# Optimization experiments

Hardware: AMD Instinct MI355X
Metric: run time of the kernel (lower is better)

## Reference

```python
import jax, jax.numpy as jnp
import numpy as np

B, L, D, G = 4, 4096, 2048, 32
GS = D // G  # group size
EPS = 1e-05


def setup_inputs() -> dict:
    key = jax.random.key(0)
    kx, = jax.random.split(key, 1)
    return {
        "x": jax.random.normal(kx, (B, L, D), dtype=jnp.float32),
        "prev_count": jnp.zeros((B,), dtype=jnp.int32),
        "prev_mean": jnp.zeros((B, G), dtype=jnp.float32),
        "prev_var": jnp.ones((B, G), dtype=jnp.float32),
        "padding_mask": jnp.ones((B, L), dtype=jnp.bool_),
        "weight": jnp.ones((D,), dtype=jnp.float32),
        "bias": jnp.zeros((D,), dtype=jnp.float32),
    }


def _timestep_norm(x, prev_count, prev_mean, prev_var, padding_mask, weight, bias):
    b, l, d = x.shape
    xg = x.reshape(b, l, G, GS).transpose(1, 0, 2, 3)  # (L, B, G, GS)
    mk = padding_mask.transpose(1, 0)                   # (L, B)
    w = weight.reshape(1, G, GS)
    bi = bias.reshape(1, G, GS)

    def step(carry, inp):
        count, mean, var = carry            # (B,), (B,G), (B,G)
        x_t, mask_t = inp                   # (B,G,GS), (B,)
        m_t = x_t.mean(axis=-1)             # per-group mean at this timestep, (B,G)
        valid = mask_t.astype(jnp.float32)[:, None]
        c_new = count + mask_t.astype(count.dtype)
        c_safe = jnp.maximum(c_new, 1).astype(jnp.float32)[:, None]
        delta = m_t - mean
        mean = mean + delta * valid / c_safe
        m2 = var * jnp.maximum(count, 1).astype(jnp.float32)[:, None]
        m2 = m2 + delta * (m_t - mean) * valid  # Welford second-moment update
        var = m2 / c_safe
        x_hat = (x_t - mean[..., None]) * jax.lax.rsqrt(var[..., None] + EPS)
        y_t = x_hat * w + bi
        return (c_new, mean, var), y_t

    (count, mean, var), ys = jax.lax.scan(step, (prev_count, prev_mean, prev_var), (xg, mk))
    y = ys.transpose(1, 0, 2, 3).reshape(b, l, d)
    return y, count, mean, var


def reference(x, prev_count, prev_mean, prev_var, padding_mask, weight, bias):
    return _timestep_norm(x, prev_count, prev_mean, prev_var, padding_mask, weight, bias)
```

## Files before the change

kernel.cpp:

```cpp
#include <hip/hip_runtime.h>

namespace {
constexpr int Bc  = 4;
constexpr int Lc  = 4096;
constexpr int Dc  = 2048;
constexpr int Gc  = 32;
constexpr int GSc = 64;
constexpr int CH  = 16;
constexpr int CT  = Lc / CH;
constexpr float EPSc = 1e-5f;
constexpr long long NY = (long long)Bc * Lc * Dc;
constexpr long long NM = (long long)Bc * Gc * Lc;
typedef float vfloat4 __attribute__((ext_vector_type(4)));
}

__global__ __launch_bounds__(256) void kA(const float* __restrict__ x,
                                          const int* __restrict__ mask,
                                          float* __restrict__ gmeans,
                                          double* __restrict__ part) {
    const int blk = blockIdx.x, chunk = blk & (CH - 1), bg = blk >> 4;
    const int b = bg >> 5, g = bg & (Gc - 1);
    const int tid = threadIdx.x, rseg = tid >> 4, col4 = tid & 15;
    const long long xbase = ((long long)b * Lc + (long long)chunk * CT) * Dc
                            + (long long)g * GSc + col4 * 4;
    const int* mrow = mask + (long long)b * Lc + chunk * CT;
    float* grow = gmeans + (long long)bg * Lc + chunk * CT;

    double ls1 = 0.0, ls2 = 0.0; int lc = 0;
    for (int it = 0; it < CT / 16; ++it) {
        const int r = it * 16 + rseg;
        const float4 xv = *reinterpret_cast<const float4*>(x + xbase + (long long)r * Dc);
        float s = xv.x + xv.y + xv.z + xv.w;
        s += __shfl_xor(s, 1);
        s += __shfl_xor(s, 2);
        s += __shfl_xor(s, 4);
        s += __shfl_xor(s, 8);
        s *= (1.0f / GSc);
        if (col4 == 0) {
            grow[r] = s;
            if (mrow[r]) { ls1 += s; ls2 += (double)s * s; ++lc; }
        }
    }
    __shared__ double a1[16], a2[16];
    __shared__ int    ac[16];
    if (col4 == 0) { a1[rseg] = ls1; a2[rseg] = ls2; ac[rseg] = lc; }
    __syncthreads();
    if (tid == 0) {
        double t1 = 0.0, t2 = 0.0; int tc = 0;
        for (int i = 0; i < 16; ++i) { t1 += a1[i]; t2 += a2[i]; tc += ac[i]; }
        double* p = part + (long long)(bg * CH + chunk) * 3;
        p[0] = t1; p[1] = t2; p[2] = (double)tc;
    }
}

__global__ __launch_bounds__(256) void kB(const float* __restrict__ x,
                                          const float* __restrict__ gmeans,
                                          const double* __restrict__ part,
                                          const int* __restrict__ prev_count,
                                          const float* __restrict__ prev_mean,
                                          const float* __restrict__ prev_var,
                                          const int* __restrict__ mask,
                                          const float* __restrict__ w,
                                          const float* __restrict__ bias,
                                          float* __restrict__ y,
                                          float* __restrict__ out_count,
                                          float* __restrict__ out_mean,
                                          float* __restrict__ out_var) {
    const int blk = blockIdx.x, chunk = blk & (CH - 1), bg = blk >> 4;
    const int b = bg >> 5, g = bg & (Gc - 1);
    const int tid = threadIdx.x;

    __shared__ float  smean[CT], srstd[CT];
    __shared__ double wt1[4], wt2[4];
    __shared__ int    wtc[4];
    __shared__ double cLDS[3];

    const float v = gmeans[(long long)bg * Lc + chunk * CT + tid];
    const int   q = mask[(long long)b * Lc + chunk * CT + tid];
    const double l1 = q ? (double)v : 0.0;
    const double l2 = q ? (double)v * v : 0.0;
    const int    lcnt = q ? 1 : 0;

    const int lane = tid & 63, wvi = tid >> 6;
    double i1 = l1, i2 = l2; int ic = lcnt;
    #pragma unroll
    for (int off = 1; off < 64; off <<= 1) {
        double t1 = __shfl_up(i1, off);
        double t2 = __shfl_up(i2, off);
        int    tc = __shfl_up(ic, off);
        if (lane >= off) { i1 += t1; i2 += t2; ic += tc; }
    }
    if (lane == 63) { wt1[wvi] = i1; wt2[wvi] = i2; wtc[wvi] = ic; }
    __syncthreads();

    if (tid < 16) {
        double a1 = 0.0, a2 = 0.0, acnt = 0.0;
        if (tid < chunk) {
            const double* p = part + (long long)(bg * CH + tid) * 3;
            a1 = p[0]; a2 = p[1]; acnt = p[2];
        }
        #pragma unroll
        for (int o = 1; o < 16; o <<= 1) {
            a1 += __shfl_xor(a1, o);
            a2 += __shfl_xor(a2, o);
            acnt += __shfl_xor(acnt, o);
        }
        if (tid == 0) { cLDS[0] = a1; cLDS[1] = a2; cLDS[2] = acnt; }
    }
    __syncthreads();

    double o1 = cLDS[0], o2 = cLDS[1], oc = cLDS[2];
    #pragma unroll
    for (int w2 = 0; w2 < 3; ++w2) {
        if (w2 < wvi) { o1 += wt1[w2]; o2 += wt2[w2]; oc += (double)wtc[w2]; }
    }
    const double run1 = o1 + i1, run2 = o2 + i2, runc = oc + (double)ic;

    const double c0    = (double)prev_count[b];
    const double mean0 = (double)prev_mean[bg];
    const double M2_0  = (double)prev_var[bg] * fmax(c0, 1.0);
    const float c0f = (float)c0, mean0f = (float)mean0, M2_0f = (float)M2_0;
    {
        float run1f = (float)run1, run2f = (float)run2, cv = (float)runc;
        float ctot = c0f + cv, csafe = fmaxf(ctot, 1.0f);
        float invcs = __builtin_amdgcn_rcpf(csafe);
        float meanT = fmaf(c0f, mean0f, run1f) * invcs;
        float M2 = M2_0f;
        if (runc > 0.0) {
            float invcv = __builtin_amdgcn_rcpf(cv);
            M2 += run2f - run1f * run1f * invcv;
            float dd = run1f * invcv - mean0f;
            M2 += dd * dd * c0f * cv * invcs;
        }
        smean[tid] = meanT;
        srstd[tid] = __builtin_amdgcn_rsqf(M2 * invcs + EPSc);
    }

    if (chunk == CH - 1 && tid == CT - 1) {
        double ctot = c0 + runc, csafe = fmax(ctot, 1.0);
        double meanF = (c0 * mean0 + run1) / csafe;
        double M2 = M2_0;
        if (runc > 0.0) {
            M2 += run2 - run1 * run1 / runc;
            double dd = run1 / runc - mean0;
            M2 += dd * dd * c0 * runc / csafe;
        }
        if (g == 0) out_count[b] = (float)ctot;
        out_mean[bg] = (float)meanF;
        out_var[bg]  = (float)(M2 / csafe);
    }
    __syncthreads();

    const int rseg = tid >> 4, col4 = tid & 15;
    const long long xbase = ((long long)b * Lc + (long long)chunk * CT) * Dc
                            + (long long)g * GSc + col4 * 4;
    const float4 wv4 = *reinterpret_cast<const float4*>(w + g * GSc + col4 * 4);
    const float4 bv4 = *reinterpret_cast<const float4*>(bias + g * GSc + col4 * 4);
    for (int it = 0; it < CT / 16; ++it) {
        const int r = it * 16 + rseg;
        const float mean = smean[r];
        const float rstd = srstd[r];
        const float4 xv = *reinterpret_cast<const float4*>(x + xbase + (long long)r * Dc);
        vfloat4 yv;
        yv.x = (xv.x - mean) * rstd * wv4.x + bv4.x;
        yv.y = (xv.y - mean) * rstd * wv4.y + bv4.y;
        yv.z = (xv.z - mean) * rstd * wv4.z + bv4.z;
        yv.w = (xv.w - mean) * rstd * wv4.w + bv4.w;
        __builtin_nontemporal_store(
            yv, reinterpret_cast<vfloat4*>(y + xbase + (long long)r * Dc));
    }
}

extern "C" void kernel_launch(void* const* d_in, const int* in_sizes, int n_in,
                              void* d_out, int out_size, void* d_ws, size_t ws_size,
                              hipStream_t stream) {
    const float* x         = (const float*)d_in[0];
    const int* prev_count  = (const int*)d_in[1];
    const float* prev_mean = (const float*)d_in[2];
    const float* prev_var  = (const float*)d_in[3];
    const int* mask        = (const int*)d_in[4];
    const float* weight    = (const float*)d_in[5];
    const float* bias      = (const float*)d_in[6];

    float* out       = (float*)d_out;
    float* y         = out;
    float* out_count = out + NY;
    float* out_mean  = out_count + Bc;
    float* out_var   = out_mean + (long long)Bc * Gc;

    float* gmeans = (float*)d_ws;
    double* part  = (double*)((char*)d_ws + NM * sizeof(float));

    const int grid = Bc * Gc * CH;
    kA<<<grid, 256, 0, stream>>>(x, mask, gmeans, part);
    kB<<<grid, 256, 0, stream>>>(x, gmeans, part, prev_count, prev_mean, prev_var,
                                 mask, weight, bias, y, out_count, out_mean, out_var);
}
```

Measured before the change: 69.65 us.

## Halve chunk count, reverse kB block order, and stage kA means in LDS

Cuts the number of time chunks from 16 to 8, so each block covers 512 timesteps and each kB thread handles two timesteps. kB blocks now run in reverse group order, so the slices of x that kA read last are normalized first, while they may still sit in cache. kA stages per-row means in LDS, writes them out as vectorized stores, and reduces the partial sums with a tree. The trade-off is fewer blocks, which lowers parallelism, and more LDS reduction steps in kA.

```diff
diff --git a/kernel.cpp b/kernel.cpp
--- a/kernel.cpp
+++ b/kernel.cpp
@@ -6,7 +6,7 @@
 constexpr int Dc  = 2048;
 constexpr int Gc  = 32;
 constexpr int GSc = 64;
-constexpr int CH  = 16;
+constexpr int CH  = 8;
 constexpr int CT  = Lc / CH;
 constexpr float EPSc = 1e-5f;
 constexpr long long NY = (long long)Bc * Lc * Dc;
@@ -18,38 +18,47 @@
                                           const int* __restrict__ mask,
                                           float* __restrict__ gmeans,
                                           double* __restrict__ part) {
-    const int blk = blockIdx.x, chunk = blk & (CH - 1), bg = blk >> 4;
+    const int blk = blockIdx.x, chunk = blk & (CH - 1), bg = blk >> 3;
     const int b = bg >> 5, g = bg & (Gc - 1);
-    const int tid = threadIdx.x, rseg = tid >> 4, col4 = tid & 15;
+    const int tid = threadIdx.x, rowi = tid >> 4, col4 = tid & 15;
     const long long xbase = ((long long)b * Lc + (long long)chunk * CT) * Dc
-                            + (long long)g * GSc + col4 * 4;
-    const int* mrow = mask + (long long)b * Lc + chunk * CT;
-    float* grow = gmeans + (long long)bg * Lc + chunk * CT;
-
-    double ls1 = 0.0, ls2 = 0.0; int lc = 0;
+                            + (long long)g * GSc;
+
+    __shared__ float sm[CT];
     for (int it = 0; it < CT / 16; ++it) {
-        const int r = it * 16 + rseg;
-        const float4 xv = *reinterpret_cast<const float4*>(x + xbase + (long long)r * Dc);
+        const int r = it * 16 + rowi;
+        const float4 xv = *reinterpret_cast<const float4*>(x + xbase + (long long)r * Dc + col4 * 4);
         float s = xv.x + xv.y + xv.z + xv.w;
         s += __shfl_xor(s, 1);
         s += __shfl_xor(s, 2);
         s += __shfl_xor(s, 4);
         s += __shfl_xor(s, 8);
-        s *= (1.0f / GSc);
-        if (col4 == 0) {
-            grow[r] = s;
-            if (mrow[r]) { ls1 += s; ls2 += (double)s * s; ++lc; }
-        }
-    }
-    __shared__ double a1[16], a2[16];
-    __shared__ int    ac[16];
-    if (col4 == 0) { a1[rseg] = ls1; a2[rseg] = ls2; ac[rseg] = lc; }
-    __syncthreads();
+        if (col4 == 0) sm[r] = s * (1.0f / GSc);
+    }
+    __syncthreads();
+
+    if (tid < CT / 4) {
+        float4 mv = *reinterpret_cast<float4*>(sm + tid * 4);
+        *reinterpret_cast<float4*>(gmeans + (long long)bg * Lc + chunk * CT + tid * 4) = mv;
+    }
+
+    const int* mrow = mask + (long long)b * Lc + chunk * CT;
+    const float v0 = sm[tid * 2], v1 = sm[tid * 2 + 1];
+    const int q0 = mrow[tid * 2], q1 = mrow[tid * 2 + 1];
+    double ls1 = 0.0, ls2 = 0.0; int lc = 0;
+    if (q0) { ls1 += v0; ls2 += (double)v0 * v0; ++lc; }
+    if (q1) { ls1 += v1; ls2 += (double)v1 * v1; ++lc; }
+    __shared__ double r1[256], r2[256];
+    __shared__ int rc[256];
+    r1[tid] = ls1; r2[tid] = ls2; rc[tid] = lc;
+    __syncthreads();
+    for (int off = 128; off > 0; off >>= 1) {
+        if (tid < off) { r1[tid] += r1[tid + off]; r2[tid] += r2[tid + off]; rc[tid] += rc[tid + off]; }
+        __syncthreads();
+    }
     if (tid == 0) {
-        double t1 = 0.0, t2 = 0.0; int tc = 0;
-        for (int i = 0; i < 16; ++i) { t1 += a1[i]; t2 += a2[i]; tc += ac[i]; }
         double* p = part + (long long)(bg * CH + chunk) * 3;
-        p[0] = t1; p[1] = t2; p[2] = (double)tc;
+        p[0] = r1[0]; p[1] = r2[0]; p[2] = (double)rc[0];
     }
 }
 
@@ -66,23 +75,28 @@
                                           float* __restrict__ out_count,
                                           float* __restrict__ out_mean,
                                           float* __restrict__ out_var) {
-    const int blk = blockIdx.x, chunk = blk & (CH - 1), bg = blk >> 4;
+    const int i = blockIdx.x;
+    const int blk2 = (Bc * Gc * CH - 8 - (i & ~7)) + (i & 7);
+    const int chunk = blk2 & (CH - 1), bg = blk2 >> 3;
     const int b = bg >> 5, g = bg & (Gc - 1);
     const int tid = threadIdx.x;
+    const int lane = tid & 63, wvi = tid >> 6;
 
     __shared__ float  smean[CT], srstd[CT];
     __shared__ double wt1[4], wt2[4];
     __shared__ int    wtc[4];
     __shared__ double cLDS[3];
 
-    const float v = gmeans[(long long)bg * Lc + chunk * CT + tid];
-    const int   q = mask[(long long)b * Lc + chunk * CT + tid];
-    const double l1 = q ? (double)v : 0.0;
-    const double l2 = q ? (double)v * v : 0.0;
-    const int    lcnt = q ? 1 : 0;
-
-    const int lane = tid & 63, wvi = tid >> 6;
-    double i1 = l1, i2 = l2; int ic = lcnt;
+    const float2 vv = *reinterpret_cast<const float2*>(gmeans + (long long)bg * Lc + chunk * CT + 2 * tid);
+    const int2   qq = *reinterpret_cast<const int2*>(mask + (long long)b * Lc + chunk * CT + 2 * tid);
+    const double e10 = qq.x ? (double)vv.x : 0.0;
+    const double e20 = qq.x ? (double)vv.x * vv.x : 0.0;
+    const double e11 = qq.y ? (double)vv.y : 0.0;
+    const double e21 = qq.y ? (double)vv.y * vv.y : 0.0;
+    const int    ec  = (qq.x ? 1 : 0) + (qq.y ? 1 : 0);
+    const double P1 = e10 + e11, P2 = e20 + e21;
+
+    double i1 = P1, i2 = P2; int ic = ec;
     #pragma unroll
     for (int off = 1; off < 64; off <<= 1) {
         double t1 = __shfl_up(i1, off);
@@ -91,16 +105,15 @@
         if (lane >= off) { i1 += t1; i2 += t2; ic += tc; }
     }
     if (lane == 63) { wt1[wvi] = i1; wt2[wvi] = i2; wtc[wvi] = ic; }
-    __syncthreads();
-
-    if (tid < 16) {
+
+    if (tid < 8) {
         double a1 = 0.0, a2 = 0.0, acnt = 0.0;
         if (tid < chunk) {
             const double* p = part + (long long)(bg * CH + tid) * 3;
             a1 = p[0]; a2 = p[1]; acnt = p[2];
         }
         #pragma unroll
-        for (int o = 1; o < 16; o <<= 1) {
+        for (int o = 1; o < 8; o <<= 1) {
             a1 += __shfl_xor(a1, o);
             a2 += __shfl_xor(a2, o);
             acnt += __shfl_xor(acnt, o);
@@ -114,13 +127,17 @@
     for (int w2 = 0; w2 < 3; ++w2) {
         if (w2 < wvi) { o1 += wt1[w2]; o2 += wt2[w2]; oc += (double)wtc[w2]; }
     }
-    const double run1 = o1 + i1, run2 = o2 + i2, runc = oc + (double)ic;
+    double run1 = o1 + (i1 - P1), run2 = o2 + (i2 - P2), runc = oc + (double)(ic - ec);
 
     const double c0    = (double)prev_count[b];
     const double mean0 = (double)prev_mean[bg];
     const double M2_0  = (double)prev_var[bg] * fmax(c0, 1.0);
     const float c0f = (float)c0, mean0f = (float)mean0, M2_0f = (float)M2_0;
-    {
+    #pragma unroll
+    for (int e = 0; e < 2; ++e) {
+        run1 += e ? e11 : e10;
+        run2 += e ? e21 : e20;
+        runc += (e ? (qq.y ? 1.0 : 0.0) : (qq.x ? 1.0 : 0.0));
         float run1f = (float)run1, run2f = (float)run2, cv = (float)runc;
         float ctot = c0f + cv, csafe = fmaxf(ctot, 1.0f);
         float invcs = __builtin_amdgcn_rcpf(csafe);
@@ -132,11 +149,11 @@
             float dd = run1f * invcv - mean0f;
             M2 += dd * dd * c0f * cv * invcs;
         }
-        smean[tid] = meanT;
-        srstd[tid] = __builtin_amdgcn_rsqf(M2 * invcs + EPSc);
-    }
-
-    if (chunk == CH - 1 && tid == CT - 1) {
+        smean[2 * tid + e] = meanT;
+        srstd[2 * tid + e] = __builtin_amdgcn_rsqf(M2 * invcs + EPSc);
+    }
+
+    if (chunk == CH - 1 && tid == 255) {
         double ctot = c0 + runc, csafe = fmax(ctot, 1.0);
         double meanF = (c0 * mean0 + run1) / csafe;
         double M2 = M2_0;
```

After: 65.07 us. 1.07x faster.
